# Performance work log

Hardware: AMD Instinct MI355X
Metric: run time of the kernel (lower is better)

The kernel has to match this reference:

```python
import jax, jax.numpy as jnp
import numpy as np

N, E, D = 100000, 1_600_000, 128  # nodes, edges, channels (in=hidden=out)


def setup_inputs() -> dict:
    key = jax.random.key(0)
    ks = jax.random.split(key, 12)
    x = jax.random.normal(ks[0], (N, D), jnp.float32)
    edge_index = jax.random.randint(ks[1], (2, E), 0, N, dtype=jnp.int32)
    def w(k):
        return jax.random.normal(k, (D, D), jnp.float32) * 0.05
    return {
        "x": x,
        "edge_index": edge_index,
        "W1": w(ks[2]), "b1": jnp.zeros((D,), jnp.float32),
        "g1": jnp.ones((D,), jnp.float32), "beta1": jnp.zeros((D,), jnp.float32),
        "W2": w(ks[3]), "b2": jnp.zeros((D,), jnp.float32),
        "g2": jnp.ones((D,), jnp.float32), "beta2": jnp.zeros((D,), jnp.float32),
        "W3": w(ks[4]), "b3": jnp.zeros((D,), jnp.float32),
    }


def gcn_conv(x, W, b, src, dst, n):
    """PyG GCNConv: h = W x, then D^{-1/2}(A+I)D^{-1/2} h + b (self-loops added)."""
    h = x @ W.T  # [N, D]
    # in-degree at destination, +1 for the implicit self-loop
    deg = jax.ops.segment_sum(jnp.ones(src.shape[0], h.dtype), dst, num_segments=n) + 1.0
    dinv = jax.lax.rsqrt(deg)  # [N]
    norm = dinv[src] * dinv[dst]  # [E]
    agg = jax.ops.segment_sum(h[src] * norm[:, None], dst, num_segments=n)
    agg = agg + h * (dinv * dinv)[:, None]  # self-loop contribution dinv_i^2 * h_i
    return agg + b


def batchnorm(x, g, b, eps=1e-5):
    # nn.BatchNorm1d in training mode: batch mean, biased variance
    mu = x.mean(axis=0)
    var = x.var(axis=0)
    return (x - mu) * jax.lax.rsqrt(var + eps) * g + b


def reference(x, edge_index, W1, b1, g1, beta1, W2, b2, g2, beta2, W3, b3):
    src, dst = edge_index[0], edge_index[1]
    n = x.shape[0]
    h = gcn_conv(x, W1, b1, src, dst, n)
    h = jax.nn.relu(batchnorm(h, g1, beta1))  # dropout p=0.0 -> identity
    h = gcn_conv(h, W2, b2, src, dst, n)
    h = jax.nn.relu(batchnorm(h, g2, beta2))
    return gcn_conv(h, W3, b3, src, dst, n)
```

## Files before the change

kernel.cpp:

```cpp
#include <hip/hip_runtime.h>

typedef __bf16 bf16x8 __attribute__((ext_vector_type(8)));
typedef float f32x4 __attribute__((ext_vector_type(4)));
typedef unsigned int uintx4 __attribute__((ext_vector_type(4)));

#define PTILE 4096
#define CSRCAP 5120

__device__ __forceinline__ float bflo(unsigned int u) { return __uint_as_float(u << 16); }
__device__ __forceinline__ float bfhi(unsigned int u) { return __uint_as_float(u & 0xffff0000u); }
__device__ __forceinline__ unsigned int f2bf(float f) {
    unsigned int u = __float_as_uint(f);
    return (u + 0x7fffu + ((u >> 16) & 1u)) >> 16;
}
__device__ __forceinline__ unsigned int pack2(float lo, float hi) {
    return (f2bf(hi) << 16) | f2bf(lo);
}

__global__ void k_cvt_w(const float* __restrict__ W1, const float* __restrict__ W2,
                        const float* __restrict__ W3, unsigned short* __restrict__ wb1,
                        unsigned short* __restrict__ wb2, unsigned short* __restrict__ wb3) {
    int i = blockIdx.x * blockDim.x + threadIdx.x;
    if (i < 128 * 128) {
        wb1[i] = (unsigned short)f2bf(W1[i]);
        wb2[i] = (unsigned short)f2bf(W2[i]);
        wb3[i] = (unsigned short)f2bf(W3[i]);
    }
}

__global__ void k_init(int* __restrict__ bktcnt, float* __restrict__ pS,
                       float* __restrict__ pQ, int NB) {
    int t = threadIdx.x;
    if (t < NB) bktcnt[t] = 0;
    for (int i = t; i < 4096; i += 512) { pS[i] = 0.f; pQ[i] = 0.f; }
}

__global__ __launch_bounds__(256) void k_bhist(const int* __restrict__ dst,
                                               int* __restrict__ bktcnt, int E, int NB) {
    __shared__ int h[512];
    for (int i = threadIdx.x; i < NB; i += 256) h[i] = 0;
    __syncthreads();
    for (int e = blockIdx.x * blockDim.x + threadIdx.x; e < E; e += gridDim.x * blockDim.x)
        atomicAdd(&h[dst[e] >> 8], 1);
    __syncthreads();
    for (int i = threadIdx.x; i < NB; i += 256) {
        int c = h[i];
        if (c) atomicAdd(&bktcnt[i], c);
    }
}

__global__ void k_scan(const int* __restrict__ bktcnt, int* __restrict__ bktoff,
                       int* __restrict__ bktcur, int NB) {
    __shared__ int s[512];
    int t = threadIdx.x;
    int v = (t < NB) ? bktcnt[t] : 0;
    s[t] = v;
    __syncthreads();
    for (int off = 1; off < 512; off <<= 1) {
        int a = (t >= off) ? s[t - off] : 0;
        __syncthreads();
        s[t] += a;
        __syncthreads();
    }
    if (t <= NB) {
        int e = s[t] - v;
        bktoff[t] = e;
        if (t < NB) bktcur[t] = e;
    }
}

__global__ __launch_bounds__(256) void k_part(const int* __restrict__ src,
                                              const int* __restrict__ dst,
                                              int* __restrict__ bktcur,
                                              unsigned long long* __restrict__ pairs,
                                              int E, int NB) {
    __shared__ int hist[512], sc[512], base[512], gbase[512];
    __shared__ unsigned long long buf[PTILE];
    int t = threadIdx.x;
    int e0 = blockIdx.x * PTILE;
    int n = min(PTILE, E - e0);

    for (int i = t; i < 512; i += 256) hist[i] = 0;
    __syncthreads();

    int mys[16], myd[16], myb[16], myr[16];
#pragma unroll
    for (int k = 0; k < 16; ++k) {
        int i = t + k * 256;
        bool ok = i < n;
        int d = ok ? dst[e0 + i] : 0;
        int s2 = ok ? src[e0 + i] : 0;
        int b = d >> 8;
        mys[k] = s2; myd[k] = d; myb[k] = b;
        myr[k] = ok ? atomicAdd(&hist[b], 1) : 0;
    }
    __syncthreads();
    sc[t] = hist[t];
    sc[t + 256] = hist[t + 256];
    __syncthreads();
    for (int off = 1; off < 512; off <<= 1) {
        int a = (t >= off) ? sc[t - off] : 0;
        int b2 = (t + 256 >= off) ? sc[t + 256 - off] : 0;
        __syncthreads();
        sc[t] += a;
        sc[t + 256] += b2;
        __syncthreads();
    }
    for (int i = t; i < NB; i += 256) {
        int c = hist[i];
        base[i] = sc[i] - c;
        gbase[i] = c ? atomicAdd(&bktcur[i], c) : 0;
    }
    __syncthreads();
#pragma unroll
    for (int k = 0; k < 16; ++k) {
        int i = t + k * 256;
        if (i < n)
            buf[base[myb[k]] + myr[k]] =
                ((unsigned long long)myd[k] << 32) | (unsigned int)mys[k];
    }
    __syncthreads();
    for (int i = t; i < n; i += 256) {
        unsigned long long p = buf[i];
        int b = (int)(p >> 40);
        pairs[gbase[b] + (i - base[b])] = p;
    }
}

__global__ __launch_bounds__(256) void k_build(const unsigned long long* __restrict__ pairs,
                                               const int* __restrict__ bktoff,
                                               int* __restrict__ counts,
                                               int* __restrict__ rowstart,
                                               float* __restrict__ dinv,
                                               int* __restrict__ csr, int N) {
    int b = blockIdx.x, t = threadIdx.x;
    int lo = bktoff[b], hi = bktoff[b + 1], m = hi - lo;
    int node0 = b << 8;
    __shared__ int cnt[256], sc2[256], cur[256];
    __shared__ int csrbuf[CSRCAP];
    cnt[t] = 0;
    __syncthreads();
    for (int i = t; i < m; i += 256) atomicAdd(&cnt[(int)(pairs[lo + i] >> 32) - node0], 1);
    __syncthreads();
    sc2[t] = cnt[t];
    __syncthreads();
    for (int off = 1; off < 256; off <<= 1) {
        int a = (t >= off) ? sc2[t - off] : 0;
        __syncthreads();
        sc2[t] += a;
        __syncthreads();
    }
    int excl = sc2[t] - cnt[t];
    int node = node0 + t;
    if (node < N) {
        counts[node] = cnt[t];
        rowstart[node] = lo + excl;
        dinv[node] = rsqrtf((float)cnt[t] + 1.0f);
    }
    cur[t] = excl;
    __syncthreads();
    if (m <= CSRCAP) {
        for (int i = t; i < m; i += 256) {
            unsigned long long p = pairs[lo + i];
            int r = atomicAdd(&cur[(int)(p >> 32) - node0], 1);
            csrbuf[r] = (int)(unsigned int)p;
        }
        __syncthreads();
        for (int i = t; i < m; i += 256) csr[lo + i] = csrbuf[i];
    } else {
        for (int i = t; i < m; i += 256) {
            unsigned long long p = pairs[lo + i];
            int r = atomicAdd(&cur[(int)(p >> 32) - node0], 1);
            csr[lo + r] = (int)(unsigned int)p;
        }
    }
}

template <int MODE>
__global__ __launch_bounds__(256) void k_gemm(const void* __restrict__ Ain,
                                              const unsigned short* __restrict__ Wb,
                                              const float* __restrict__ dinv,
                                              const float* __restrict__ bnA,
                                              const float* __restrict__ bnB,
                                              unsigned short* __restrict__ hs, int N) {
    int wv = threadIdx.x >> 6;
    int lane = threadIdx.x & 63;
    int ln = lane & 15, hi = lane >> 4;
    int rowbase = blockIdx.x * 64 + wv * 16;
    int arow = rowbase + ln;
    bool aok = arow < N;

    bf16x8 a[4];
#pragma unroll
    for (int kc = 0; kc < 4; ++kc) {
        int kb = kc * 32 + hi * 8;
        unsigned int w2[4];
        if (MODE == 0) {
            const float4* Ap = (const float4*)((const float*)Ain + (size_t)arow * 128 + kb);
            float4 f0 = aok ? Ap[0] : make_float4(0.f, 0.f, 0.f, 0.f);
            float4 f1 = aok ? Ap[1] : make_float4(0.f, 0.f, 0.f, 0.f);
            w2[0] = pack2(f0.x, f0.y);
            w2[1] = pack2(f0.z, f0.w);
            w2[2] = pack2(f1.x, f1.y);
            w2[3] = pack2(f1.z, f1.w);
        } else {
            const uintx4* Ap =
                (const uintx4*)((const unsigned short*)Ain + (size_t)arow * 128 + kb);
            uintx4 zz = {0u, 0u, 0u, 0u};
            uintx4 u = aok ? Ap[0] : zz;
#pragma unroll
            for (int j = 0; j < 4; ++j) {
                int c = kb + 2 * j;
                float lo = fmaxf(bflo(u[j]) * bnA[c] + bnB[c], 0.f);
                float h2 = fmaxf(bfhi(u[j]) * bnA[c + 1] + bnB[c + 1], 0.f);
                w2[j] = pack2(lo, h2);
            }
        }
        uintx4 uu = {w2[0], w2[1], w2[2], w2[3]};
        a[kc] = __builtin_bit_cast(bf16x8, uu);
    }

    float dv[4];
    int er0 = rowbase + hi * 4;
#pragma unroll
    for (int q = 0; q < 4; ++q) dv[q] = (er0 + q < N) ? dinv[er0 + q] : 0.f;

#pragma unroll
    for (int ct = 0; ct < 8; ++ct) {
        int col = ct * 16 + ln;
        const uintx4* Wp = (const uintx4*)(Wb + col * 128 + hi * 8);
        f32x4 acc = {0.f, 0.f, 0.f, 0.f};
#pragma unroll
        for (int kc = 0; kc < 4; ++kc) {
            bf16x8 bfr = __builtin_bit_cast(bf16x8, Wp[kc * 4]);
            acc = __builtin_amdgcn_mfma_f32_16x16x32_bf16(a[kc], bfr, acc, 0, 0, 0);
        }
#pragma unroll
        for (int q = 0; q < 4; ++q) {
            int r = er0 + q;
            if (r < N) hs[(size_t)r * 128 + col] = (unsigned short)f2bf(acc[q] * dv[q]);
        }
    }
}

template <int FINAL>
__global__ __launch_bounds__(256) void k_gather(const unsigned int* __restrict__ hs2,
                                                const int* __restrict__ csr,
                                                const int* __restrict__ rowstart,
                                                const int* __restrict__ counts,
                                                const float* __restrict__ dinv,
                                                unsigned int* __restrict__ pre2,
                                                float* __restrict__ outf,
                                                const float* __restrict__ bias,
                                                float* __restrict__ pS,
                                                float* __restrict__ pQ, int N) {
    int lane = threadIdx.x & 63;
    int w = blockIdx.x * 4 + (threadIdx.x >> 6);
    int nw = gridDim.x * 4;
    float ws0 = 0.f, ws1 = 0.f, wq0 = 0.f, wq1 = 0.f;

    for (int i = w; i < N; i += nw) {
        int st = rowstart[i], cnt = counts[i];
        unsigned int us = hs2[(size_t)i * 64 + lane];
        float s0 = bflo(us), s1 = bfhi(us);

        if (cnt <= 64) {
            int idx = (lane < cnt) ? csr[st + lane] : 0;
            int nfull = cnt & ~7;
            if (nfull) {
                int e[8];
                unsigned int u[8];
#pragma unroll
                for (int k = 0; k < 8; ++k) e[k] = __shfl(idx, k, 64);
#pragma unroll
                for (int k = 0; k < 8; ++k) u[k] = hs2[(size_t)e[k] * 64 + lane];
                for (int j = 8; j < nfull; j += 8) {
                    int en[8];
                    unsigned int un[8];
#pragma unroll
                    for (int k = 0; k < 8; ++k) en[k] = __shfl(idx, j + k, 64);
#pragma unroll
                    for (int k = 0; k < 8; ++k) un[k] = hs2[(size_t)en[k] * 64 + lane];
#pragma unroll
                    for (int k = 0; k < 8; ++k) { s0 += bflo(u[k]); s1 += bfhi(u[k]); }
#pragma unroll
                    for (int k = 0; k < 8; ++k) u[k] = un[k];
                }
#pragma unroll
                for (int k = 0; k < 8; ++k) { s0 += bflo(u[k]); s1 += bfhi(u[k]); }
            }
            for (int j = nfull; j < cnt; ++j) {
                int e0 = __shfl(idx, j, 64);
                unsigned int u = hs2[(size_t)e0 * 64 + lane];
                s0 += bflo(u);
                s1 += bfhi(u);
            }
        } else {
            for (int j = 0; j < cnt; ++j) {
                unsigned int u = hs2[(size_t)csr[st + j] * 64 + lane];
                s0 += bflo(u);
                s1 += bfhi(u);
            }
        }

        float sc = dinv[i];
        s0 *= sc;
        s1 *= sc;
        if (FINAL) {
            float2 o;
            o.x = s0 + bias[2 * lane];
            o.y = s1 + bias[2 * lane + 1];
            ((float2*)outf)[(size_t)i * 64 + lane] = o;
        } else {
            pre2[(size_t)i * 64 + lane] = pack2(s0, s1);
            ws0 += s0; ws1 += s1;
            wq0 += s0 * s0; wq1 += s1 * s1;
        }
    }

    if (!FINAL) {
        __shared__ float red[4][64][4];
        int h = threadIdx.x >> 6;
        red[h][lane][0] = ws0; red[h][lane][1] = ws1;
        red[h][lane][2] = wq0; red[h][lane][3] = wq1;
        __syncthreads();
        if (h == 0) {
#pragma unroll
            for (int hh = 1; hh < 4; ++hh) {
                ws0 += red[hh][lane][0]; ws1 += red[hh][lane][1];
                wq0 += red[hh][lane][2]; wq1 += red[hh][lane][3];
            }
            int slot = (blockIdx.x & 31) * 128;
            atomicAdd(&pS[slot + 2 * lane], ws0);
            atomicAdd(&pS[slot + 2 * lane + 1], ws1);
            atomicAdd(&pQ[slot + 2 * lane], wq0);
            atomicAdd(&pQ[slot + 2 * lane + 1], wq1);
        }
    }
}

__global__ void k_bnfin(const float* __restrict__ g, const float* __restrict__ beta,
                        float* __restrict__ pS, float* __restrict__ pQ,
                        float* __restrict__ bnA, float* __restrict__ bnB, float invN) {
    int c = threadIdx.x;
    if (c < 128) {
        float s = 0.f, q = 0.f;
        for (int k = 0; k < 32; ++k) {
            s += pS[k * 128 + c]; q += pQ[k * 128 + c];
            pS[k * 128 + c] = 0.f; pQ[k * 128 + c] = 0.f;
        }
        float m = s * invN;
        float var = q * invN - m * m;
        float istd = rsqrtf(var + 1e-5f);
        float A = g[c] * istd;
        bnA[c] = A;
        bnB[c] = beta[c] - m * A;
    }
}

extern "C" void kernel_launch(void* const* d_in, const int* in_sizes, int n_in,
                              void* d_out, int out_size, void* d_ws, size_t ws_size,
                              hipStream_t stream) {
    const float* x = (const float*)d_in[0];
    const int* ei = (const int*)d_in[1];
    const float* W1 = (const float*)d_in[2];
    const float* g1 = (const float*)d_in[4];
    const float* be1 = (const float*)d_in[5];
    const float* W2 = (const float*)d_in[6];
    const float* g2 = (const float*)d_in[8];
    const float* be2 = (const float*)d_in[9];
    const float* W3 = (const float*)d_in[10];
    const float* b3 = (const float*)d_in[11];

    int N = in_sizes[0] / 128;
    int E = in_sizes[1] / 2;
    int NB = (N + 255) >> 8;
    const int* srcp = ei;
    const int* dstp = ei + E;

    char* w = (char*)d_ws;
    auto alloc = [&](size_t b) { char* p = w; w += (b + 255) & ~(size_t)255; return p; };
    int* counts = (int*)alloc((size_t)N * 4);
    int* rowstart = (int*)alloc((size_t)N * 4);
    float* dinv = (float*)alloc((size_t)N * 4);
    int* bktcnt = (int*)alloc(2048);
    int* bktoff = (int*)alloc(2048 + 4);
    int* bktcur = (int*)alloc(2048);
    float* pS = (float*)alloc(4096 * 4);
    float* pQ = (float*)alloc(4096 * 4);
    float* bnA = (float*)alloc(512);
    float* bnB = (float*)alloc(512);
    int* csr = (int*)alloc((size_t)E * 4);
    unsigned long long* pairs = (unsigned long long*)alloc((size_t)E * 8);
    unsigned short* wb1 = (unsigned short*)alloc(16384 * 2);
    unsigned short* wb2 = (unsigned short*)alloc(16384 * 2);
    unsigned short* wb3 = (unsigned short*)alloc(16384 * 2);
    unsigned short* hs = (unsigned short*)alloc((size_t)N * 128 * 2);
    unsigned short* pre = (unsigned short*)alloc((size_t)N * 128 * 2);
    (void)ws_size; (void)n_in; (void)out_size;

    int gemm_grid = (N + 63) / 64;
    int npart = (E + PTILE - 1) / PTILE;
    float invN = 1.0f / (float)N;

    k_init<<<1, 512, 0, stream>>>(bktcnt, pS, pQ, NB);
    k_cvt_w<<<64, 256, 0, stream>>>(W1, W2, W3, wb1, wb2, wb3);
    k_bhist<<<256, 256, 0, stream>>>(dstp, bktcnt, E, NB);
    k_scan<<<1, 512, 0, stream>>>(bktcnt, bktoff, bktcur, NB);
    k_part<<<npart, 256, 0, stream>>>(srcp, dstp, bktcur, pairs, E, NB);
    k_build<<<NB, 256, 0, stream>>>(pairs, bktoff, counts, rowstart, dinv, csr, N);

    k_gemm<0><<<gemm_grid, 256, 0, stream>>>(x, wb1, dinv, nullptr, nullptr, hs, N);
    k_gather<0><<<2048, 256, 0, stream>>>((const unsigned int*)hs, csr, rowstart, counts, dinv,
                                          (unsigned int*)pre, nullptr, nullptr, pS, pQ, N);
    k_bnfin<<<1, 128, 0, stream>>>(g1, be1, pS, pQ, bnA, bnB, invN);
    k_gemm<1><<<gemm_grid, 256, 0, stream>>>(pre, wb2, dinv, bnA, bnB, hs, N);
    k_gather<0><<<2048, 256, 0, stream>>>((const unsigned int*)hs, csr, rowstart, counts, dinv,
                                          (unsigned int*)pre, nullptr, nullptr, pS, pQ, N);
    k_bnfin<<<1, 128, 0, stream>>>(g2, be2, pS, pQ, bnA, bnB, invN);
    k_gemm<1><<<gemm_grid, 256, 0, stream>>>(pre, wb3, dinv, bnA, bnB, hs, N);
    k_gather<1><<<2048, 256, 0, stream>>>((const unsigned int*)hs, csr, rowstart, counts, dinv,
                                          nullptr, (float*)d_out, b3, nullptr, nullptr, N);
}
```

Before: 370.3 us.

## Slice feature matrices into 16-channel column blocks for cache-local gather

```diff
diff --git a/kernel.cpp b/kernel.cpp
--- a/kernel.cpp
+++ b/kernel.cpp
@@ -129,8 +129,7 @@
 
 __global__ __launch_bounds__(256) void k_build(const unsigned long long* __restrict__ pairs,
                                                const int* __restrict__ bktoff,
-                                               int* __restrict__ counts,
-                                               int* __restrict__ rowstart,
+                                               int2* __restrict__ rc,
                                                float* __restrict__ dinv,
                                                int* __restrict__ csr, int N) {
     int b = blockIdx.x, t = threadIdx.x;
@@ -153,8 +152,7 @@
     int excl = sc2[t] - cnt[t];
     int node = node0 + t;
     if (node < N) {
-        counts[node] = cnt[t];
-        rowstart[node] = lo + excl;
+        rc[node] = make_int2(lo + excl, cnt[t]);
         dinv[node] = rsqrtf((float)cnt[t] + 1.0f);
     }
     cur[t] = excl;
@@ -204,10 +202,11 @@
             w2[2] = pack2(f1.x, f1.y);
             w2[3] = pack2(f1.z, f1.w);
         } else {
-            const uintx4* Ap =
-                (const uintx4*)((const unsigned short*)Ain + (size_t)arow * 128 + kb);
+            const uintx4* Ap = (const uintx4*)((const unsigned int*)Ain +
+                                               ((size_t)(kb >> 4) * N + arow) * 8 +
+                                               ((kb >> 1) & 7));
             uintx4 zz = {0u, 0u, 0u, 0u};
-            uintx4 u = aok ? Ap[0] : zz;
+            uintx4 u = aok ? *Ap : zz;
 #pragma unroll
             for (int j = 0; j < 4; ++j) {
                 int c = kb + 2 * j;
@@ -238,103 +237,106 @@
 #pragma unroll
         for (int q = 0; q < 4; ++q) {
             int r = er0 + q;
-            if (r < N) hs[(size_t)r * 128 + col] = (unsigned short)f2bf(acc[q] * dv[q]);
+            if (r < N) hs[((size_t)ct * N + r) * 16 + ln] = (unsigned short)f2bf(acc[q] * dv[q]);
         }
     }
 }
 
 template <int FINAL>
-__global__ __launch_bounds__(256) void k_gather(const unsigned int* __restrict__ hs2,
+__global__ __launch_bounds__(256) void k_gather(const unsigned int* __restrict__ hsS,
+                                                const int2* __restrict__ rc,
                                                 const int* __restrict__ csr,
-                                                const int* __restrict__ rowstart,
-                                                const int* __restrict__ counts,
                                                 const float* __restrict__ dinv,
-                                                unsigned int* __restrict__ pre2,
+                                                unsigned int* __restrict__ preS,
                                                 float* __restrict__ outf,
                                                 const float* __restrict__ bias,
                                                 float* __restrict__ pS,
                                                 float* __restrict__ pQ, int N) {
     int lane = threadIdx.x & 63;
-    int w = blockIdx.x * 4 + (threadIdx.x >> 6);
-    int nw = gridDim.x * 4;
+    int wv = threadIdx.x >> 6;
+    int slice = blockIdx.x & 7;
+    int gblk = blockIdx.x >> 3;
+    int w = gblk * 4 + wv;
+    int nw = (gridDim.x >> 3) * 4;
+    int sub = lane >> 3, cl = lane & 7;
+    const unsigned int* hb = hsS + (size_t)slice * N * 8;
+
+    float bx = 0.f, by = 0.f;
+    if (FINAL) {
+        bx = bias[slice * 16 + 2 * cl];
+        by = bias[slice * 16 + 2 * cl + 1];
+    }
     float ws0 = 0.f, ws1 = 0.f, wq0 = 0.f, wq1 = 0.f;
 
     for (int i = w; i < N; i += nw) {
-        int st = rowstart[i], cnt = counts[i];
-        unsigned int us = hs2[(size_t)i * 64 + lane];
-        float s0 = bflo(us), s1 = bfhi(us);
-
-        if (cnt <= 64) {
-            int idx = (lane < cnt) ? csr[st + lane] : 0;
-            int nfull = cnt & ~7;
-            if (nfull) {
-                int e[8];
-                unsigned int u[8];
-#pragma unroll
-                for (int k = 0; k < 8; ++k) e[k] = __shfl(idx, k, 64);
-#pragma unroll
-                for (int k = 0; k < 8; ++k) u[k] = hs2[(size_t)e[k] * 64 + lane];
-                for (int j = 8; j < nfull; j += 8) {
-                    int en[8];
-                    unsigned int un[8];
-#pragma unroll
-                    for (int k = 0; k < 8; ++k) en[k] = __shfl(idx, j + k, 64);
-#pragma unroll
-                    for (int k = 0; k < 8; ++k) un[k] = hs2[(size_t)en[k] * 64 + lane];
-#pragma unroll
-                    for (int k = 0; k < 8; ++k) { s0 += bflo(u[k]); s1 += bfhi(u[k]); }
-#pragma unroll
-                    for (int k = 0; k < 8; ++k) u[k] = un[k];
-                }
-#pragma unroll
-                for (int k = 0; k < 8; ++k) { s0 += bflo(u[k]); s1 += bfhi(u[k]); }
-            }
-            for (int j = nfull; j < cnt; ++j) {
-                int e0 = __shfl(idx, j, 64);
-                unsigned int u = hs2[(size_t)e0 * 64 + lane];
-                s0 += bflo(u);
-                s1 += bfhi(u);
-            }
+        int2 rcv = rc[i];
+        int st = rcv.x, cnt = rcv.y;
+        unsigned int us = hb[(size_t)i * 8 + cl];
+        float s0 = (sub == 0) ? bflo(us) : 0.f;
+        float s1 = (sub == 0) ? bfhi(us) : 0.f;
+
+#define GBATCH(b)                                                   \
+    {                                                               \
+        int j = ((b) << 3) + sub;                                   \
+        bool v = j < cnt;                                           \
+        int e = v ? csr[st + j] : 0;                                \
+        unsigned int u = v ? hb[(size_t)e * 8 + cl] : 0u;           \
+        s0 += bflo(u);                                              \
+        s1 += bfhi(u);                                              \
+    }
+        int nb = (cnt + 7) >> 3;
+        if (nb <= 2) {
+            GBATCH(0); GBATCH(1);
+        } else if (nb <= 4) {
+            GBATCH(0); GBATCH(1); GBATCH(2); GBATCH(3);
         } else {
-            for (int j = 0; j < cnt; ++j) {
-                unsigned int u = hs2[(size_t)csr[st + j] * 64 + lane];
-                s0 += bflo(u);
-                s1 += bfhi(u);
-            }
-        }
-
+            for (int b = 0; b < nb; ++b) GBATCH(b);
+        }
+#undef GBATCH
+
+#pragma unroll
+        for (int m = 8; m < 64; m <<= 1) {
+            s0 += __shfl_xor(s0, m, 64);
+            s1 += __shfl_xor(s1, m, 64);
+        }
         float sc = dinv[i];
         s0 *= sc;
         s1 *= sc;
+
         if (FINAL) {
-            float2 o;
-            o.x = s0 + bias[2 * lane];
-            o.y = s1 + bias[2 * lane + 1];
-            ((float2*)outf)[(size_t)i * 64 + lane] = o;
+            if (sub == 0) {
+                float2 o;
+                o.x = s0 + bx;
+                o.y = s1 + by;
+                ((float2*)outf)[(size_t)i * 64 + slice * 8 + cl] = o;
+            }
         } else {
-            pre2[(size_t)i * 64 + lane] = pack2(s0, s1);
+            if (sub == 0) preS[((size_t)slice * N + i) * 8 + cl] = pack2(s0, s1);
             ws0 += s0; ws1 += s1;
             wq0 += s0 * s0; wq1 += s1 * s1;
         }
     }
 
     if (!FINAL) {
-        __shared__ float red[4][64][4];
-        int h = threadIdx.x >> 6;
-        red[h][lane][0] = ws0; red[h][lane][1] = ws1;
-        red[h][lane][2] = wq0; red[h][lane][3] = wq1;
-        __syncthreads();
-        if (h == 0) {
-#pragma unroll
-            for (int hh = 1; hh < 4; ++hh) {
-                ws0 += red[hh][lane][0]; ws1 += red[hh][lane][1];
-                wq0 += red[hh][lane][2]; wq1 += red[hh][lane][3];
+        __shared__ float red[4][8][4];
+        if (sub == 0) {
+            red[wv][cl][0] = ws0; red[wv][cl][1] = ws1;
+            red[wv][cl][2] = wq0; red[wv][cl][3] = wq1;
+        }
+        __syncthreads();
+        if (threadIdx.x < 8) {
+            int c = threadIdx.x;
+            float a0 = 0.f, a1 = 0.f, a2 = 0.f, a3 = 0.f;
+#pragma unroll
+            for (int hh = 0; hh < 4; ++hh) {
+                a0 += red[hh][c][0]; a1 += red[hh][c][1];
+                a2 += red[hh][c][2]; a3 += red[hh][c][3];
             }
-            int slot = (blockIdx.x & 31) * 128;
-            atomicAdd(&pS[slot + 2 * lane], ws0);
-            atomicAdd(&pS[slot + 2 * lane + 1], ws1);
-            atomicAdd(&pQ[slot + 2 * lane], wq0);
-            atomicAdd(&pQ[slot + 2 * lane + 1], wq1);
+            int base = (gblk & 31) * 128 + slice * 16 + 2 * c;
+            atomicAdd(&pS[base], a0);
+            atomicAdd(&pS[base + 1], a1);
+            atomicAdd(&pQ[base], a2);
+            atomicAdd(&pQ[base + 1], a3);
         }
     }
 }
@@ -380,8 +382,7 @@
 
     char* w = (char*)d_ws;
     auto alloc = [&](size_t b) { char* p = w; w += (b + 255) & ~(size_t)255; return p; };
-    int* counts = (int*)alloc((size_t)N * 4);
-    int* rowstart = (int*)alloc((size_t)N * 4);
+    int2* rc = (int2*)alloc((size_t)N * 8);
     float* dinv = (float*)alloc((size_t)N * 4);
     int* bktcnt = (int*)alloc(2048);
     int* bktoff = (int*)alloc(2048 + 4);
@@ -408,17 +409,17 @@
     k_bhist<<<256, 256, 0, stream>>>(dstp, bktcnt, E, NB);
     k_scan<<<1, 512, 0, stream>>>(bktcnt, bktoff, bktcur, NB);
     k_part<<<npart, 256, 0, stream>>>(srcp, dstp, bktcur, pairs, E, NB);
-    k_build<<<NB, 256, 0, stream>>>(pairs, bktoff, counts, rowstart, dinv, csr, N);
+    k_build<<<NB, 256, 0, stream>>>(pairs, bktoff, rc, dinv, csr, N);
 
     k_gemm<0><<<gemm_grid, 256, 0, stream>>>(x, wb1, dinv, nullptr, nullptr, hs, N);
-    k_gather<0><<<2048, 256, 0, stream>>>((const unsigned int*)hs, csr, rowstart, counts, dinv,
+    k_gather<0><<<2048, 256, 0, stream>>>((const unsigned int*)hs, rc, csr, dinv,
                                           (unsigned int*)pre, nullptr, nullptr, pS, pQ, N);
     k_bnfin<<<1, 128, 0, stream>>>(g1, be1, pS, pQ, bnA, bnB, invN);
     k_gemm<1><<<gemm_grid, 256, 0, stream>>>(pre, wb2, dinv, bnA, bnB, hs, N);
-    k_gather<0><<<2048, 256, 0, stream>>>((const unsigned int*)hs, csr, rowstart, counts, dinv,
+    k_gather<0><<<2048, 256, 0, stream>>>((const unsigned int*)hs, rc, csr, dinv,
                                           (unsigned int*)pre, nullptr, nullptr, pS, pQ, N);
     k_bnfin<<<1, 128, 0, stream>>>(g2, be2, pS, pQ, bnA, bnB, invN);
     k_gemm<1><<<gemm_grid, 256, 0, stream>>>(pre, wb3, dinv, bnA, bnB, hs, N);
-    k_gather<1><<<2048, 256, 0, stream>>>((const unsigned int*)hs, csr, rowstart, counts, dinv,
-                                          nullptr, (float*)d_out, b3, nullptr, nullptr, N);
-}
+    k_gather<1><<<2048, 256, 0, stream>>>((const unsigned int*)hs, rc, csr, dinv, nullptr,
+                                          (float*)d_out, b3, nullptr, nullptr, N);
+}
```

New measurement: 697.6 us. +88.4%, slower.
